# Kernel tuning notes

Measured on AMD Instinct MI355X. Metric: run time of the kernel, lower is better.

Reference implementation:

```python
import jax, jax.numpy as jnp
import numpy as np

N = 50000
E = 800000
C = 64
NEG_SLOPE = 0.2


def gat_conv(x, edge_index, W, att_src, att_dst, bias, heads, out_ch):
    """PyG GATConv forward (concat=True, add_self_loops=True).
    x: [N, in], edge_index: [2, E] (row0=src j, row1=dst i),
    W: [in, heads*out_ch], att_src/att_dst: [heads, out_ch], bias: [heads*out_ch].
    """
    n = x.shape[0]
    loop = jnp.arange(n, dtype=edge_index.dtype)
    src = jnp.concatenate([edge_index[0], loop])
    dst = jnp.concatenate([edge_index[1], loop])

    xl = (x @ W).reshape(n, heads, out_ch)            # [N, H, F]
    a_src = jnp.einsum('nhf,hf->nh', xl, att_src)      # [N, H]
    a_dst = jnp.einsum('nhf,hf->nh', xl, att_dst)      # [N, H]

    alpha = jax.nn.leaky_relu(a_src[src] + a_dst[dst], NEG_SLOPE)  # [E', H]
    # segment softmax over incoming edges of each destination node
    amax = jax.ops.segment_max(alpha, dst, num_segments=n)
    alpha = jnp.exp(alpha - amax[dst])
    denom = jax.ops.segment_sum(alpha, dst, num_segments=n)
    alpha = alpha / denom[dst]

    # gather source features, weight, scatter-add to destinations
    msg = xl[src] * alpha[:, :, None]                  # [E', H, F]
    out = jax.ops.segment_sum(msg, dst, num_segments=n)  # [N, H, F]
    return out.reshape(n, heads * out_ch) + bias


def setup_inputs() -> dict:
    key = jax.random.key(0)
    ks = jax.random.split(key, 12)
    x = jax.random.normal(ks[0], (N, C), dtype=jnp.float32)
    undirected = jax.random.randint(ks[1], (2, E), 0, N, dtype=jnp.int32)
    directed = jax.random.randint(ks[2], (2, E), 0, N, dtype=jnp.int32)

    s1 = 1.0 / np.sqrt(C)
    s2 = 1.0 / np.sqrt(2 * C)
    W1 = jax.random.normal(ks[3], (C, 2 * C), dtype=jnp.float32) * s1
    att_src1 = jax.random.normal(ks[4], (2, C), dtype=jnp.float32) * s1
    att_dst1 = jax.random.normal(ks[5], (2, C), dtype=jnp.float32) * s1
    b1 = jnp.zeros((2 * C,), dtype=jnp.float32)

    W2 = jax.random.normal(ks[6], (2 * C, 4 * C), dtype=jnp.float32) * s2
    att_src2 = jax.random.normal(ks[7], (2, 2 * C), dtype=jnp.float32) * s2
    att_dst2 = jax.random.normal(ks[8], (2, 2 * C), dtype=jnp.float32) * s2
    b2 = jnp.zeros((4 * C,), dtype=jnp.float32)

    return {
        'x': x,
        'undirected_edges_small': undirected,
        'directed_edges_small': directed,
        'W1': W1, 'att_src1': att_src1, 'att_dst1': att_dst1, 'b1': b1,
        'W2': W2, 'att_src2': att_src2, 'att_dst2': att_dst2, 'b2': b2,
    }


def reference(x, undirected_edges_small, directed_edges_small,
              W1, att_src1, att_dst1, b1,
              W2, att_src2, att_dst2, b2):
    h = gat_conv(x, undirected_edges_small, W1, att_src1, att_dst1, b1,
                 heads=2, out_ch=C)            # [N, 2C]
    out = gat_conv(h, directed_edges_small, W2, att_src2, att_dst2, b2,
                   heads=2, out_ch=2 * C)      # [N, 4C]
    return out
```

## Files before the change

### kernel.cpp

```cpp
#include <hip/hip_runtime.h>
#include <stdint.h>

#define N_NODES 50000
#define N_EDGES 800000
#define CAP 64
#define NBUCK 400
#define BSZ 125
#define BCAP 2816
#define LOG2E 1.4426950408889634f

typedef __attribute__((ext_vector_type(8))) short bf16x8;
typedef __attribute__((ext_vector_type(4))) float f32x4;

__device__ __forceinline__ float b2f_bits(unsigned int lo16) {
    union { unsigned int i; float f; } v; v.i = lo16 << 16; return v.f;
}
__device__ __forceinline__ unsigned short f2b(float f) {
    union { float f; unsigned int i; } v; v.f = f;
    unsigned int x = v.i;
    return (unsigned short)((x + 0x7fffu + ((x >> 16) & 1u)) >> 16);
}
__device__ __forceinline__ void split2(float v, unsigned short& h, unsigned short& l) {
    h = f2b(v);
    l = f2b(v - b2f_bits(h));
}
__device__ __forceinline__ void unpack8(const uint4 u, float* f) {
    f[0] = b2f_bits(u.x & 0xffffu); f[1] = b2f_bits(u.x >> 16);
    f[2] = b2f_bits(u.y & 0xffffu); f[3] = b2f_bits(u.y >> 16);
    f[4] = b2f_bits(u.z & 0xffffu); f[5] = b2f_bits(u.z >> 16);
    f[6] = b2f_bits(u.w & 0xffffu); f[7] = b2f_bits(u.w >> 16);
}
__device__ __forceinline__ void pack8hl(const float* v, uint4& H, uint4& L) {
    unsigned short h[8], l[8];
#pragma unroll
    for (int k = 0; k < 8; ++k) split2(v[k], h[k], l[k]);
    H.x = h[0] | ((unsigned)h[1] << 16); H.y = h[2] | ((unsigned)h[3] << 16);
    H.z = h[4] | ((unsigned)h[5] << 16); H.w = h[6] | ((unsigned)h[7] << 16);
    L.x = l[0] | ((unsigned)l[1] << 16); L.y = l[2] | ((unsigned)l[3] << 16);
    L.z = l[4] | ((unsigned)l[5] << 16); L.w = l[6] | ((unsigned)l[7] << 16);
}

__global__ __launch_bounds__(256) void proj_kernel(
    const float* __restrict__ W1, const float* __restrict__ as1, const float* __restrict__ ad1,
    const float* __restrict__ b1,
    const float* __restrict__ W2, const float* __restrict__ as2, const float* __restrict__ ad2,
    float* __restrict__ P1, float* __restrict__ q2, float* __restrict__ cs,
    int* __restrict__ gcur)
{
    for (int i = threadIdx.x; i < 2 * NBUCK + 2; i += 256) gcur[i] = 0;

    __shared__ float p2[4 * 128];
    for (int i = threadIdx.x; i < 4 * 128; i += 256) {
        const int t = i >> 7, c = i & 127;
        const int h = t & 1;
        const float* att = (t < 2) ? as2 : ad2;
        float s = 0.f;
        for (int cc = 0; cc < 128; ++cc)
            s += att[h * 128 + cc] * W2[(size_t)c * 256 + h * 128 + cc];
        p2[i] = s;
    }
    {
        const int t = threadIdx.x >> 6, k = threadIdx.x & 63;
        const int h = t & 1;
        const float* att = (t < 2) ? as1 : ad1;
        float s = 0.f;
        for (int c = 0; c < 64; ++c)
            s += att[h * 64 + c] * W1[(size_t)k * 128 + h * 64 + c];
        P1[t * 64 + k] = s * LOG2E;
    }
    __syncthreads();
    for (int i = threadIdx.x; i < 4 * 128; i += 256) {
        const int t = i >> 7, j = i & 127;
        const int hc = j >> 6, k = j & 63;
        float s = 0.f;
        for (int c = 0; c < 64; ++c)
            s += W1[(size_t)k * 128 + hc * 64 + c] * p2[t * 128 + hc * 64 + c];
        q2[i] = s * LOG2E;
    }
    if (threadIdx.x < 4) {
        const int t = threadIdx.x;
        float s = 0.f;
        for (int c = 0; c < 128; ++c) s += b1[c] * p2[t * 128 + c];
        cs[t] = s * LOG2E;
    }
}

__global__ __launch_bounds__(256) void prep1_kernel(
    const float* __restrict__ X, const float* __restrict__ P1,
    const float* __restrict__ W1, const float* __restrict__ W2,
    unsigned short* __restrict__ Xh,
    float* __restrict__ a_src, float* __restrict__ a_dst,
    unsigned short* __restrict__ w1h, unsigned short* __restrict__ w1l,
    unsigned short* __restrict__ w2h, unsigned short* __restrict__ w2l,
    float* __restrict__ att2buf, int n)
{
    const int bid = blockIdx.x;
    if (bid < 128) {
        const int i = bid * 256 + threadIdx.x;
        const int nn = i >> 7, k = i & 127;
        unsigned short h, l;
        split2(W2[(size_t)k * 256 + nn], h, l);
        w2h[i] = h; w2l[i] = l;
        return;
    }
    if (bid < 160) {
        const int i = (bid - 128) * 256 + threadIdx.x;
        const int nn = i >> 6, k = i & 63;
        unsigned short h, l;
        split2(W1[(size_t)k * 128 + nn], h, l);
        w1h[i] = h; w1l[i] = l;
        return;
    }
    const int gid = (bid - 160) * 256 + threadIdx.x;
    if (gid < n) ((float4*)att2buf)[gid] = make_float4(0.f, 0.f, 0.f, 0.f);
    const int node = gid >> 4;
    const int sl = threadIdx.x & 15;
    if (node >= n) return;
    const float4 v = *(const float4*)(X + (size_t)node * 64 + sl * 4);
    ushort4 hv;
    hv.x = f2b(v.x); hv.y = f2b(v.y); hv.z = f2b(v.z); hv.w = f2b(v.w);
    *(ushort4*)(Xh + (size_t)node * 64 + sl * 4) = hv;
    float d[4];
#pragma unroll
    for (int t = 0; t < 4; ++t) {
        const float* pp = P1 + t * 64 + sl * 4;
        d[t] = v.x * pp[0] + v.y * pp[1] + v.z * pp[2] + v.w * pp[3];
    }
#pragma unroll
    for (int o = 1; o < 16; o <<= 1)
#pragma unroll
        for (int t = 0; t < 4; ++t) d[t] += __shfl_xor(d[t], o);
    if (sl == 0) {
        *(float2*)(a_src + node * 2) = make_float2(d[0], d[1]);
        *(float2*)(a_dst + node * 2) = make_float2(d[2], d[3]);
    }
}

__global__ __launch_bounds__(256) void bucket_kernel(
    const int* __restrict__ e1, const int* __restrict__ e2, int ne,
    int* __restrict__ gcur, unsigned int* __restrict__ stage)
{
    const int layer = blockIdx.x & 1;
    const int bslot = blockIdx.x >> 1;
    const int nbl = gridDim.x >> 1;
    const int* __restrict__ eix = layer ? e2 : e1;
    int* cur = gcur + layer * NBUCK;
    unsigned int* __restrict__ stg = stage + (size_t)layer * NBUCK * BCAP;

    __shared__ int cnt_lds[NBUCK];
    __shared__ int base_lds[NBUCK];
    constexpr int EPT = 16;
    constexpr int CHUNK = 256 * EPT;

    for (int base = bslot * CHUNK; base < ne; base += nbl * CHUNK) {
        for (int i = threadIdx.x; i < NBUCK; i += 256) cnt_lds[i] = 0;
        __syncthreads();

        unsigned int rec[EPT];
        int bk[EPT];
#pragma unroll
        for (int i = 0; i < EPT; ++i) {
            const int e = base + i * 256 + threadIdx.x;
            bk[i] = -1;
            if (e < ne) {
                const int s = eix[e];
                const int d = eix[ne + e];
                if ((unsigned)d < (unsigned)N_NODES) {
                    const int b = d / BSZ;
                    bk[i] = b;
                    rec[i] = (unsigned)s | ((unsigned)(d - b * BSZ) << 16);
                    atomicAdd(&cnt_lds[b], 1);
                }
            }
        }
        __syncthreads();
        for (int i = threadIdx.x; i < NBUCK; i += 256) {
            const int c = cnt_lds[i];
            base_lds[i] = c ? atomicAdd(&cur[i], c) : 0;
            cnt_lds[i] = 0;
        }
        __syncthreads();
#pragma unroll
        for (int i = 0; i < EPT; ++i) {
            if (bk[i] >= 0) {
                const int idx = base_lds[bk[i]] + atomicAdd(&cnt_lds[bk[i]], 1);
                if (idx < BCAP) stg[(size_t)bk[i] * BCAP + idx] = rec[i];
            }
        }
        __syncthreads();
    }
}

__global__ __launch_bounds__(256) void place_kernel(
    const unsigned int* __restrict__ stage, const int* __restrict__ gcur,
    int* __restrict__ gtot,
    unsigned int* __restrict__ offs1, unsigned int* __restrict__ offs2,
    unsigned short* __restrict__ ss1, unsigned short* __restrict__ ss2)
{
    const int layer = blockIdx.x & 1;
    const int bucket = blockIdx.x >> 1;
    int m = gcur[layer * NBUCK + bucket];
    m = m < BCAP ? m : BCAP;
    const unsigned int* __restrict__ stg =
        stage + ((size_t)(layer * NBUCK + bucket)) * BCAP;
    unsigned int* __restrict__ offs = layer ? offs2 : offs1;
    unsigned short* __restrict__ ss = layer ? ss2 : ss1;
    const int d0 = bucket * BSZ;

    __shared__ int c_lds[BSZ];
    __shared__ int pref[BSZ + 1];
    __shared__ int baseSh;
    __shared__ unsigned short img[BCAP];

    for (int i = threadIdx.x; i < BSZ; i += 256) c_lds[i] = 0;
    __syncthreads();

    for (int i = threadIdx.x; i < m; i += 256)
        atomicAdd(&c_lds[stg[i] >> 16], 1);
    __syncthreads();

    if (threadIdx.x == 0) {
        int run = 0;
        for (int i = 0; i < BSZ; ++i) {
            int c = c_lds[i]; c = c < CAP ? c : CAP;
            pref[i] = run; run += c;
        }
        pref[BSZ] = run;
        baseSh = atomicAdd(&gtot[layer], run);
    }
    __syncthreads();
    const int base = baseSh;
    for (int i = threadIdx.x; i < BSZ; i += 256) {
        int c = c_lds[i]; c = c < CAP ? c : CAP;
        offs[d0 + i] = ((unsigned)(base + pref[i]) << 7) | (unsigned)c;
        c_lds[i] = 0;
    }
    __syncthreads();

    for (int i = threadIdx.x; i < m; i += 256) {
        const unsigned int v = stg[i];
        const int dr = (int)(v >> 16);
        const int slot = atomicAdd(&c_lds[dr], 1);
        if (slot < CAP) img[pref[dr] + slot] = (unsigned short)(v & 0xffffu);
    }
    __syncthreads();

    unsigned short* out = ss + base;
    const int tot = pref[BSZ];
    for (int i = threadIdx.x; i < tot; i += 256) out[i] = img[i];
}

__global__ __launch_bounds__(256) void agg1_kernel(
    const unsigned short* __restrict__ XH, const float* __restrict__ X,
    const float* __restrict__ a_src, const float* __restrict__ a_dst,
    const unsigned int* __restrict__ offs, const unsigned short* __restrict__ bins,
    unsigned short* __restrict__ AH, unsigned short* __restrict__ AL, int n)
{
    const int node = (blockIdx.x * 256 + threadIdx.x) >> 6;
    const int lane = threadIdx.x & 63;
    if (node >= n) return;
    const int hl = lane & 7;
    const int sub = lane >> 3;

    const unsigned o = offs[node];
    const int start = (int)(o >> 7);
    const int deg = (int)(o & 127);
    const int e = start + deg;
    const float2 ad = *(const float2*)(a_dst + node * 2);

    float2 As; float4 sva, svb;
    if (sub == 0) {
        As = *(const float2*)(a_src + node * 2);
        sva = *(const float4*)(X + (size_t)node * 64 + hl * 8);
        svb = *(const float4*)(X + (size_t)node * 64 + hl * 8 + 4);
    }

    float acc0[8] = {0.f,0.f,0.f,0.f,0.f,0.f,0.f,0.f};
    float acc1[8] = {0.f,0.f,0.f,0.f,0.f,0.f,0.f,0.f};
    float den0 = 0.f, den1 = 0.f;

    int p = start;
    int jc = 0; float2 Ac = make_float2(0.f, 0.f); uint4 uc = make_uint4(0,0,0,0);
    if (p < e) {
        const int pos = p + sub;
        const int pc = pos < e ? pos : e - 1;
        jc = bins[pc];
        Ac = *(const float2*)(a_src + jc * 2);
        uc = *(const uint4*)(XH + (size_t)jc * 64 + hl * 8);
    }
    while (p < e) {
        const int pn = p + 8;
        int jn = 0; float2 An; uint4 un;
        const bool more = pn < e;
        if (more) {
            const int pos = pn + sub;
            const int pc = pos < e ? pos : e - 1;
            jn = bins[pc];
            An = *(const float2*)(a_src + jn * 2);
            un = *(const uint4*)(XH + (size_t)jn * 64 + hl * 8);
        }
        float l0 = Ac.x + ad.x; l0 = fmaxf(l0, 0.2f * l0);
        float l1 = Ac.y + ad.y; l1 = fmaxf(l1, 0.2f * l1);
        float w0 = __builtin_amdgcn_exp2f(l0);
        float w1 = __builtin_amdgcn_exp2f(l1);
        if (p + sub >= e) { w0 = 0.f; w1 = 0.f; }
        den0 += w0; den1 += w1;
        float f[8]; unpack8(uc, f);
#pragma unroll
        for (int k = 0; k < 8; ++k) { acc0[k] += w0 * f[k]; acc1[k] += w1 * f[k]; }
        if (!more) break;
        jc = jn; Ac = An; uc = un; p = pn;
    }
    if (sub == 0) {
        float l0 = As.x + ad.x; l0 = fmaxf(l0, 0.2f * l0);
        float l1 = As.y + ad.y; l1 = fmaxf(l1, 0.2f * l1);
        const float w0 = __builtin_amdgcn_exp2f(l0);
        const float w1 = __builtin_amdgcn_exp2f(l1);
        den0 += w0; den1 += w1;
        float f[8] = {sva.x, sva.y, sva.z, sva.w, svb.x, svb.y, svb.z, svb.w};
#pragma unroll
        for (int k = 0; k < 8; ++k) { acc0[k] += w0 * f[k]; acc1[k] += w1 * f[k]; }
    }
#pragma unroll
    for (int o2 = 8; o2 < 64; o2 <<= 1) {
        den0 += __shfl_xor(den0, o2); den1 += __shfl_xor(den1, o2);
#pragma unroll
        for (int k = 0; k < 8; ++k) {
            acc0[k] += __shfl_xor(acc0[k], o2);
            acc1[k] += __shfl_xor(acc1[k], o2);
        }
    }
    if (sub < 2) {
        const int head = sub;
        const float inv = 1.f / (head ? den1 : den0);
        float vv[8];
#pragma unroll
        for (int k = 0; k < 8; ++k) vv[k] = (head ? acc1[k] : acc0[k]) * inv;
        uint4 H, L;
        pack8hl(vv, H, L);
        const size_t off = (size_t)head * N_NODES * 64 + (size_t)node * 64 + hl * 8;
        *(uint4*)(AH + off) = H;
        *(uint4*)(AL + off) = L;
    }
}

__global__ __launch_bounds__(256) void agg2_kernel(
    const unsigned short* __restrict__ HH, const unsigned short* __restrict__ HL,
    const float* __restrict__ a_src, const float* __restrict__ a_dst,
    const float* __restrict__ cs,
    const unsigned int* __restrict__ offs, const unsigned short* __restrict__ bins,
    unsigned short* __restrict__ AH, unsigned short* __restrict__ AL, int n)
{
    const int node = (blockIdx.x * 256 + threadIdx.x) >> 6;
    const int lane = threadIdx.x & 63;
    if (node >= n) return;
    const int hl = lane & 15;
    const int sub = lane >> 4;

    const float4 csv = *(const float4*)cs;
    const float C0 = csv.x + csv.z, C1 = csv.y + csv.w;

    const unsigned o = offs[node];
    const int start = (int)(o >> 7);
    const int deg = (int)(o & 127);
    const int e = start + deg;
    const float2 ad = *(const float2*)(a_dst + node * 2);
    const float ad0 = ad.x + C0, ad1 = ad.y + C1;

    float2 As; uint4 suh, sul;
    if (sub == 0) {
        As = *(const float2*)(a_src + node * 2);
        suh = *(const uint4*)(HH + (size_t)node * 128 + hl * 8);
        sul = *(const uint4*)(HL + (size_t)node * 128 + hl * 8);
    }

    float acc0[8] = {0.f,0.f,0.f,0.f,0.f,0.f,0.f,0.f};
    float acc1[8] = {0.f,0.f,0.f,0.f,0.f,0.f,0.f,0.f};
    float den0 = 0.f, den1 = 0.f;

    int p = start;
    int jc = 0; float2 Ac = make_float2(0.f, 0.f); uint4 uc = make_uint4(0,0,0,0);
    if (p < e) {
        const int pos = p + sub;
        const int pc = pos < e ? pos : e - 1;
        jc = bins[pc];
        Ac = *(const float2*)(a_src + jc * 2);
        uc = *(const uint4*)(HH + (size_t)jc * 128 + hl * 8);
    }
    while (p < e) {
        const int pn = p + 4;
        int jn = 0; float2 An; uint4 un;
        const bool more = pn < e;
        if (more) {
            const int pos = pn + sub;
            const int pc = pos < e ? pos : e - 1;
            jn = bins[pc];
            An = *(const float2*)(a_src + jn * 2);
            un = *(const uint4*)(HH + (size_t)jn * 128 + hl * 8);
        }
        float l0 = Ac.x + ad0; l0 = fmaxf(l0, 0.2f * l0);
        float l1 = Ac.y + ad1; l1 = fmaxf(l1, 0.2f * l1);
        float w0 = __builtin_amdgcn_exp2f(l0);
        float w1 = __builtin_amdgcn_exp2f(l1);
        if (p + sub >= e) { w0 = 0.f; w1 = 0.f; }
        den0 += w0; den1 += w1;
        float f[8]; unpack8(uc, f);
#pragma unroll
        for (int k = 0; k < 8; ++k) { acc0[k] += w0 * f[k]; acc1[k] += w1 * f[k]; }
        if (!more) break;
        jc = jn; Ac = An; uc = un; p = pn;
    }
    if (sub == 0) {
        float l0 = As.x + ad0; l0 = fmaxf(l0, 0.2f * l0);
        float l1 = As.y + ad1; l1 = fmaxf(l1, 0.2f * l1);
        const float w0 = __builtin_amdgcn_exp2f(l0);
        const float w1 = __builtin_amdgcn_exp2f(l1);
        den0 += w0; den1 += w1;
        float fh[8], fl[8];
        unpack8(suh, fh); unpack8(sul, fl);
#pragma unroll
        for (int k = 0; k < 8; ++k) {
            const float f = fh[k] + fl[k];
            acc0[k] += w0 * f; acc1[k] += w1 * f;
        }
    }
#pragma unroll
    for (int o2 = 16; o2 < 64; o2 <<= 1) {
        den0 += __shfl_xor(den0, o2); den1 += __shfl_xor(den1, o2);
#pragma unroll
        for (int k = 0; k < 8; ++k) {
            acc0[k] += __shfl_xor(acc0[k], o2);
            acc1[k] += __shfl_xor(acc1[k], o2);
        }
    }
    if (sub < 2) {
        const int head = sub;
        const float inv = 1.f / (head ? den1 : den0);
        float vv[8];
#pragma unroll
        for (int k = 0; k < 8; ++k) vv[k] = (head ? acc1[k] : acc0[k]) * inv;
        uint4 H, L;
        pack8hl(vv, H, L);
        const size_t off = (size_t)head * N_NODES * 128 + (size_t)node * 128 + hl * 8;
        *(uint4*)(AH + off) = H;
        *(uint4*)(AL + off) = L;
    }
}

__global__ __launch_bounds__(512) void gemm_h_kernel(
    const unsigned short* __restrict__ AH, const unsigned short* __restrict__ AL,
    const unsigned short* __restrict__ WTh, const unsigned short* __restrict__ WTl,
    const float* __restrict__ b1, const float* __restrict__ q2,
    unsigned short* __restrict__ HH, unsigned short* __restrict__ HL,
    float* __restrict__ a_src2, float* __restrict__ a_dst2, int M)
{
    constexpr int K = 64, KC = 2;
    const int wave = threadIdx.x >> 6;
    const int lane = threadIdx.x & 63;
    const int head = wave >> 2;
    const int c0 = (wave & 3) * 16;
    const int lr = lane & 15;
    const int lk = (lane >> 4) * 8;
    const int colg = head * 64 + c0 + ((lane >> 4) << 2);
    const bool doAtt = (wave & 3) == 0;

    bf16x8 awh[KC], awl[KC];
    {
        const unsigned short* wr  = WTh + (size_t)(head * 64 + c0 + lr) * K + lk;
        const unsigned short* wr2 = WTl + (size_t)(head * 64 + c0 + lr) * K + lk;
#pragma unroll
        for (int c = 0; c < KC; ++c) {
            awh[c] = *(const bf16x8*)(wr + c * 32);
            awl[c] = *(const bf16x8*)(wr2 + c * 32);
        }
    }
    const float4 bias = *(const float4*)(b1 + colg);
    const unsigned short* XhB = AH + (size_t)head * M * 64;
    const unsigned short* XlB = AL + (size_t)head * M * 64;

    auto loadB = [&](bf16x8 (&bh)[KC], bf16x8 (&bl)[KC], int sidx) {
        const unsigned short* xr  = XhB + (size_t)(sidx * 16 + lr) * 64 + lk;
        const unsigned short* xr2 = XlB + (size_t)(sidx * 16 + lr) * 64 + lk;
#pragma unroll
        for (int c = 0; c < KC; ++c) {
            bh[c] = *(const bf16x8*)(xr + c * 32);
            bl[c] = *(const bf16x8*)(xr2 + c * 32);
        }
    };
    auto compute = [&](bf16x8 (&bh)[KC], bf16x8 (&bl)[KC], int sidx) {
        f32x4 acc = {0.f, 0.f, 0.f, 0.f};
#pragma unroll
        for (int c = 0; c < KC; ++c)
            acc = __builtin_amdgcn_mfma_f32_16x16x32_bf16(awh[c], bh[c], acc, 0, 0, 0);
#pragma unroll
        for (int c = 0; c < KC; ++c)
            acc = __builtin_amdgcn_mfma_f32_16x16x32_bf16(awh[c], bl[c], acc, 0, 0, 0);
#pragma unroll
        for (int c = 0; c < KC; ++c)
            acc = __builtin_amdgcn_mfma_f32_16x16x32_bf16(awl[c], bh[c], acc, 0, 0, 0);
        ushort4 hv, lv;
        split2(acc[0] + bias.x, hv.x, lv.x); split2(acc[1] + bias.y, hv.y, lv.y);
        split2(acc[2] + bias.z, hv.z, lv.z); split2(acc[3] + bias.w, hv.w, lv.w);
        const size_t o = (size_t)(sidx * 16 + lr) * 128 + colg;
        *(ushort4*)(HH + o) = hv;
        *(ushort4*)(HL + o) = lv;
        if (doAtt) {
            float P[4] = {0.f, 0.f, 0.f, 0.f};
#pragma unroll
            for (int c = 0; c < KC; ++c)
#pragma unroll
                for (int i = 0; i < 8; ++i) {
                    const float v = b2f_bits((unsigned short)bh[c][i])
                                  + b2f_bits((unsigned short)bl[c][i]);
                    const int kk = head * 64 + lk + c * 32 + i;
#pragma unroll
                    for (int t = 0; t < 4; ++t) P[t] += v * q2[t * 128 + kk];
                }
#pragma unroll
            for (int o2 = 16; o2 < 64; o2 <<= 1)
#pragma unroll
                for (int t = 0; t < 4; ++t) P[t] += __shfl_xor(P[t], o2);
            if (lane < 16) {
                const int m = sidx * 16 + lane;
                atomicAdd(&a_src2[m * 2 + 0], P[0]);
                atomicAdd(&a_src2[m * 2 + 1], P[1]);
                atomicAdd(&a_dst2[m * 2 + 0], P[2]);
                atomicAdd(&a_dst2[m * 2 + 1], P[3]);
            }
        }
    };

    const int NSTRIP = M / 16;
    const int nb = gridDim.x;
    int s = blockIdx.x;
    bf16x8 b0h[KC], b0l[KC], b1h_[KC], b1l_[KC];
    if (s < NSTRIP) loadB(b0h, b0l, s);
    while (s < NSTRIP) {
        const int sn = s + nb;
        if (sn < NSTRIP) loadB(b1h_, b1l_, sn);
        compute(b0h, b0l, s);
        if (sn >= NSTRIP) break;
        const int sn2 = sn + nb;
        if (sn2 < NSTRIP) loadB(b0h, b0l, sn2);
        compute(b1h_, b1l_, sn);
        s = sn2;
    }
}

__global__ __launch_bounds__(512) void gemm_out_kernel(
    const unsigned short* __restrict__ AH, const unsigned short* __restrict__ AL,
    const unsigned short* __restrict__ WTh, const unsigned short* __restrict__ WTl,
    const float* __restrict__ b2,
    float* __restrict__ OUT, int M)
{
    constexpr int K = 128, KC = 4, CT = 2;
    const int wave = threadIdx.x >> 6;
    const int lane = threadIdx.x & 63;
    const int head = wave >> 2;
    const int c0 = (wave & 3) * 32;
    const int lr = lane & 15;
    const int lk = (lane >> 4) * 8;

    bf16x8 awh[CT][KC], awl[CT][KC];
    float4 bias[CT];
    int colg[CT];
#pragma unroll
    for (int t = 0; t < CT; ++t) {
        const unsigned short* wr  = WTh + (size_t)(head * 128 + c0 + t * 16 + lr) * K + lk;
        const unsigned short* wr2 = WTl + (size_t)(head * 128 + c0 + t * 16 + lr) * K + lk;
#pragma unroll
        for (int c = 0; c < KC; ++c) {
            awh[t][c] = *(const bf16x8*)(wr + c * 32);
            awl[t][c] = *(const bf16x8*)(wr2 + c * 32);
        }
        colg[t] = head * 128 + c0 + t * 16 + ((lane >> 4) << 2);
        bias[t] = *(const float4*)(b2 + colg[t]);
    }
    const unsigned short* XhB = AH + (size_t)head * M * 128;
    const unsigned short* XlB = AL + (size_t)head * M * 128;

    auto loadB = [&](bf16x8 (&bh)[KC], bf16x8 (&bl)[KC], int sidx) {
        const unsigned short* xr  = XhB + (size_t)(sidx * 16 + lr) * 128 + lk;
        const unsigned short* xr2 = XlB + (size_t)(sidx * 16 + lr) * 128 + lk;
#pragma unroll
        for (int c = 0; c < KC; ++c) {
            bh[c] = *(const bf16x8*)(xr + c * 32);
            bl[c] = *(const bf16x8*)(xr2 + c * 32);
        }
    };
    auto compute = [&](bf16x8 (&bh)[KC], bf16x8 (&bl)[KC], int sidx) {
#pragma unroll
        for (int t = 0; t < CT; ++t) {
            f32x4 acc = {0.f, 0.f, 0.f, 0.f};
#pragma unroll
            for (int c = 0; c < KC; ++c)
                acc = __builtin_amdgcn_mfma_f32_16x16x32_bf16(awh[t][c], bh[c], acc, 0, 0, 0);
#pragma unroll
            for (int c = 0; c < KC; ++c)
                acc = __builtin_amdgcn_mfma_f32_16x16x32_bf16(awh[t][c], bl[c], acc, 0, 0, 0);
#pragma unroll
            for (int c = 0; c < KC; ++c)
                acc = __builtin_amdgcn_mfma_f32_16x16x32_bf16(awl[t][c], bh[c], acc, 0, 0, 0);
            float4 o;
            o.x = acc[0] + bias[t].x; o.y = acc[1] + bias[t].y;
            o.z = acc[2] + bias[t].z; o.w = acc[3] + bias[t].w;
            *(float4*)(OUT + (size_t)(sidx * 16 + lr) * 256 + colg[t]) = o;
        }
    };

    const int NSTRIP = M / 16;
    const int nb = gridDim.x;
    int s = blockIdx.x;
    bf16x8 b0h[KC], b0l[KC], b1h_[KC], b1l_[KC];
    if (s < NSTRIP) loadB(b0h, b0l, s);
    while (s < NSTRIP) {
        const int sn = s + nb;
        if (sn < NSTRIP) loadB(b1h_, b1l_, sn);
        compute(b0h, b0l, s);
        if (sn >= NSTRIP) break;
        const int sn2 = sn + nb;
        if (sn2 < NSTRIP) loadB(b0h, b0l, sn2);
        compute(b1h_, b1l_, sn);
        s = sn2;
    }
}

extern "C" void kernel_launch(void* const* d_in, const int* in_sizes, int n_in,
                              void* d_out, int out_size, void* d_ws, size_t ws_size,
                              hipStream_t stream)
{
    const int N = N_NODES, E = N_EDGES;

    const float* x   = (const float*)d_in[0];
    const int*   und = (const int*)d_in[1];
    const int*   dir = (const int*)d_in[2];
    const float* W1  = (const float*)d_in[3];
    const float* as1 = (const float*)d_in[4];
    const float* ad1 = (const float*)d_in[5];
    const float* b1  = (const float*)d_in[6];
    const float* W2  = (const float*)d_in[7];
    const float* as2 = (const float*)d_in[8];
    const float* ad2 = (const float*)d_in[9];
    const float* b2  = (const float*)d_in[10];

    char* p = (char*)d_ws;
    auto alloc = [&](size_t bytes) {
        char* r = p;
        p += (bytes + 255) & ~(size_t)255;
        return r;
    };
    unsigned short* agg2h = (unsigned short*)alloc((size_t)2 * N * 128 * 2);
    unsigned short* agg2l = (unsigned short*)alloc((size_t)2 * N * 128 * 2);
    unsigned short* hhbuf = (unsigned short*)alloc((size_t)N * 128 * 2);
    unsigned short* hlbuf = (unsigned short*)alloc((size_t)N * 128 * 2);
    unsigned short* ss1   = (unsigned short*)alloc((size_t)E * 2);
    unsigned short* ss2   = (unsigned short*)alloc((size_t)E * 2);
    unsigned int* offs1 = (unsigned int*)alloc((size_t)N * 4);
    unsigned int* offs2 = (unsigned int*)alloc((size_t)N * 4);
    float* a_src1 = (float*)alloc((size_t)N * 2 * 4);
    float* a_dst1 = (float*)alloc((size_t)N * 2 * 4);
    float* att2buf = (float*)alloc((size_t)N * 4 * 4);
    int*   gcur  = (int*)alloc(((size_t)2 * NBUCK + 2) * 4);
    unsigned short* w1th = (unsigned short*)alloc((size_t)128 * 64 * 2);
    unsigned short* w1tl = (unsigned short*)alloc((size_t)128 * 64 * 2);
    unsigned short* w2th = (unsigned short*)alloc((size_t)256 * 128 * 2);
    unsigned short* w2tl = (unsigned short*)alloc((size_t)256 * 128 * 2);
    float* P1d = (float*)alloc(4 * 64 * 4);
    float* q2d = (float*)alloc(4 * 128 * 4);
    float* csd = (float*)alloc(4 * 4);
    int* gtot = gcur + 2 * NBUCK;
    float* a_src2 = att2buf, * a_dst2 = att2buf + (size_t)N * 2;

    unsigned int* stage = (unsigned int*)agg2h;
    unsigned short* x1h   = (unsigned short*)d_out;
    unsigned short* agg1h = (unsigned short*)d_out + (size_t)N * 64;
    unsigned short* agg1l = (unsigned short*)d_out + (size_t)N * 64 + (size_t)N * 128;

    const int WB = (N * 64) / 256;

    proj_kernel<<<1, 256, 0, stream>>>(W1, as1, ad1, b1, W2, as2, ad2,
                                       P1d, q2d, csd, gcur);
    bucket_kernel<<<2 * 196, 256, 0, stream>>>(und, dir, E, gcur, stage);
    place_kernel<<<2 * NBUCK, 256, 0, stream>>>(stage, gcur, gtot,
                                                offs1, offs2, ss1, ss2);
    prep1_kernel<<<160 + (N * 16) / 256, 256, 0, stream>>>(
        x, P1d, W1, W2, x1h, a_src1, a_dst1,
        w1th, w1tl, w2th, w2tl, att2buf, N);

    agg1_kernel<<<WB, 256, 0, stream>>>(x1h, x, a_src1, a_dst1, offs1, ss1,
                                        agg1h, agg1l, N);
    gemm_h_kernel<<<768, 512, 0, stream>>>(agg1h, agg1l, w1th, w1tl, b1, q2d,
                                           hhbuf, hlbuf, a_src2, a_dst2, N);

    agg2_kernel<<<WB, 256, 0, stream>>>(hhbuf, hlbuf, a_src2, a_dst2, csd,
                                        offs2, ss2, agg2h, agg2l, N);
    gemm_out_kernel<<<512, 512, 0, stream>>>(agg2h, agg2l, w2th, w2tl, b2,
                                             (float*)d_out, N);
}
```

Baseline: 295.8 us.

## Fuse edge aggregation with following MFMA GEMM via LDS staging per strip

Replaces the separate aggregation and GEMM kernels for both GAT layers with fused kernels. Each 512-thread block handles 16-node strips: waves aggregate two nodes each, write the hi/lo bf16 split results into swizzled LDS, then apply the weight transform with MFMA and write outputs directly. This removes the global round trip of the aggregated intermediates and two launches. In exchange it drops the software prefetch in the gather loop, adds two block barriers per strip, and moves the staging buffer to its own workspace allocation.

```diff
diff --git a/kernel.cpp b/kernel.cpp
--- a/kernel.cpp
+++ b/kernel.cpp
@@ -250,378 +250,283 @@
     for (int i = threadIdx.x; i < tot; i += 256) out[i] = img[i];
 }
 
-__global__ __launch_bounds__(256) void agg1_kernel(
+__global__ __launch_bounds__(512, 4) void fused1_kernel(
     const unsigned short* __restrict__ XH, const float* __restrict__ X,
     const float* __restrict__ a_src, const float* __restrict__ a_dst,
     const unsigned int* __restrict__ offs, const unsigned short* __restrict__ bins,
-    unsigned short* __restrict__ AH, unsigned short* __restrict__ AL, int n)
-{
-    const int node = (blockIdx.x * 256 + threadIdx.x) >> 6;
+    const unsigned short* __restrict__ WTh, const unsigned short* __restrict__ WTl,
+    const float* __restrict__ b1, const float* __restrict__ q2,
+    unsigned short* __restrict__ HH, unsigned short* __restrict__ HL,
+    float* __restrict__ a_src2, float* __restrict__ a_dst2, int nstrips)
+{
+    __shared__ __align__(16) unsigned char lds[2 * 2 * 16 * 128];
+    const int wave = threadIdx.x >> 6;
     const int lane = threadIdx.x & 63;
-    if (node >= n) return;
     const int hl = lane & 7;
     const int sub = lane >> 3;
-
-    const unsigned o = offs[node];
-    const int start = (int)(o >> 7);
-    const int deg = (int)(o & 127);
-    const int e = start + deg;
-    const float2 ad = *(const float2*)(a_dst + node * 2);
-
-    float2 As; float4 sva, svb;
-    if (sub == 0) {
-        As = *(const float2*)(a_src + node * 2);
-        sva = *(const float4*)(X + (size_t)node * 64 + hl * 8);
-        svb = *(const float4*)(X + (size_t)node * 64 + hl * 8 + 4);
-    }
-
-    float acc0[8] = {0.f,0.f,0.f,0.f,0.f,0.f,0.f,0.f};
-    float acc1[8] = {0.f,0.f,0.f,0.f,0.f,0.f,0.f,0.f};
-    float den0 = 0.f, den1 = 0.f;
-
-    int p = start;
-    int jc = 0; float2 Ac = make_float2(0.f, 0.f); uint4 uc = make_uint4(0,0,0,0);
-    if (p < e) {
-        const int pos = p + sub;
-        const int pc = pos < e ? pos : e - 1;
-        jc = bins[pc];
-        Ac = *(const float2*)(a_src + jc * 2);
-        uc = *(const uint4*)(XH + (size_t)jc * 64 + hl * 8);
-    }
-    while (p < e) {
-        const int pn = p + 8;
-        int jn = 0; float2 An; uint4 un;
-        const bool more = pn < e;
-        if (more) {
-            const int pos = pn + sub;
-            const int pc = pos < e ? pos : e - 1;
-            jn = bins[pc];
-            An = *(const float2*)(a_src + jn * 2);
-            un = *(const uint4*)(XH + (size_t)jn * 64 + hl * 8);
-        }
-        float l0 = Ac.x + ad.x; l0 = fmaxf(l0, 0.2f * l0);
-        float l1 = Ac.y + ad.y; l1 = fmaxf(l1, 0.2f * l1);
-        float w0 = __builtin_amdgcn_exp2f(l0);
-        float w1 = __builtin_amdgcn_exp2f(l1);
-        if (p + sub >= e) { w0 = 0.f; w1 = 0.f; }
-        den0 += w0; den1 += w1;
-        float f[8]; unpack8(uc, f);
-#pragma unroll
-        for (int k = 0; k < 8; ++k) { acc0[k] += w0 * f[k]; acc1[k] += w1 * f[k]; }
-        if (!more) break;
-        jc = jn; Ac = An; uc = un; p = pn;
-    }
-    if (sub == 0) {
-        float l0 = As.x + ad.x; l0 = fmaxf(l0, 0.2f * l0);
-        float l1 = As.y + ad.y; l1 = fmaxf(l1, 0.2f * l1);
-        const float w0 = __builtin_amdgcn_exp2f(l0);
-        const float w1 = __builtin_amdgcn_exp2f(l1);
-        den0 += w0; den1 += w1;
-        float f[8] = {sva.x, sva.y, sva.z, sva.w, svb.x, svb.y, svb.z, svb.w};
-#pragma unroll
-        for (int k = 0; k < 8; ++k) { acc0[k] += w0 * f[k]; acc1[k] += w1 * f[k]; }
-    }
-#pragma unroll
-    for (int o2 = 8; o2 < 64; o2 <<= 1) {
-        den0 += __shfl_xor(den0, o2); den1 += __shfl_xor(den1, o2);
-#pragma unroll
-        for (int k = 0; k < 8; ++k) {
-            acc0[k] += __shfl_xor(acc0[k], o2);
-            acc1[k] += __shfl_xor(acc1[k], o2);
-        }
-    }
-    if (sub < 2) {
-        const int head = sub;
-        const float inv = 1.f / (head ? den1 : den0);
-        float vv[8];
-#pragma unroll
-        for (int k = 0; k < 8; ++k) vv[k] = (head ? acc1[k] : acc0[k]) * inv;
-        uint4 H, L;
-        pack8hl(vv, H, L);
-        const size_t off = (size_t)head * N_NODES * 64 + (size_t)node * 64 + hl * 8;
-        *(uint4*)(AH + off) = H;
-        *(uint4*)(AL + off) = L;
-    }
-}
-
-__global__ __launch_bounds__(256) void agg2_kernel(
+    const int headC = wave >> 2;
+    const int c0 = (wave & 3) * 16;
+    const int lr = lane & 15;
+    const int lk = (lane >> 4) * 8;
+    const int colg = headC * 64 + c0 + ((lane >> 4) << 2);
+    const bool doAtt = (wave & 3) == 0;
+
+    bf16x8 awh[2], awl[2];
+    {
+        const unsigned short* wr  = WTh + (size_t)(headC * 64 + c0 + lr) * 64 + lk;
+        const unsigned short* wr2 = WTl + (size_t)(headC * 64 + c0 + lr) * 64 + lk;
+        awh[0] = *(const bf16x8*)(wr);  awh[1] = *(const bf16x8*)(wr + 32);
+        awl[0] = *(const bf16x8*)(wr2); awl[1] = *(const bf16x8*)(wr2 + 32);
+    }
+    const float4 bias = *(const float4*)(b1 + colg);
+
+    for (int strip = blockIdx.x; strip < nstrips; strip += gridDim.x) {
+#pragma unroll
+        for (int nn = 0; nn < 2; ++nn) {
+            const int node = strip * 16 + wave * 2 + nn;
+            const int ln = wave * 2 + nn;
+            const unsigned o = offs[node];
+            const int start = (int)(o >> 7);
+            const int e = start + (int)(o & 127);
+            const float2 ad = *(const float2*)(a_dst + node * 2);
+            float acc0[8] = {0,0,0,0,0,0,0,0}, acc1[8] = {0,0,0,0,0,0,0,0};
+            float den0 = 0.f, den1 = 0.f;
+            for (int p = start; p < e; p += 8) {
+                const int pos = p + sub;
+                const int pc = pos < e ? pos : e - 1;
+                const int j = bins[pc];
+                const float2 A = *(const float2*)(a_src + j * 2);
+                const uint4 u = *(const uint4*)(XH + (size_t)j * 64 + hl * 8);
+                float l0 = A.x + ad.x; l0 = fmaxf(l0, 0.2f * l0);
+                float l1 = A.y + ad.y; l1 = fmaxf(l1, 0.2f * l1);
+                float w0 = __builtin_amdgcn_exp2f(l0);
+                float w1 = __builtin_amdgcn_exp2f(l1);
+                if (pos >= e) { w0 = 0.f; w1 = 0.f; }
+                den0 += w0; den1 += w1;
+                float f[8]; unpack8(u, f);
+#pragma unroll
+                for (int k = 0; k < 8; ++k) { acc0[k] += w0 * f[k]; acc1[k] += w1 * f[k]; }
+            }
+            if (sub == 0) {
+                const float2 A = *(const float2*)(a_src + node * 2);
+                const float4 va = *(const float4*)(X + (size_t)node * 64 + hl * 8);
+                const float4 vb = *(const float4*)(X + (size_t)node * 64 + hl * 8 + 4);
+                float l0 = A.x + ad.x; l0 = fmaxf(l0, 0.2f * l0);
+                float l1 = A.y + ad.y; l1 = fmaxf(l1, 0.2f * l1);
+                const float w0 = __builtin_amdgcn_exp2f(l0);
+                const float w1 = __builtin_amdgcn_exp2f(l1);
+                den0 += w0; den1 += w1;
+                float f[8] = {va.x, va.y, va.z, va.w, vb.x, vb.y, vb.z, vb.w};
+#pragma unroll
+                for (int k = 0; k < 8; ++k) { acc0[k] += w0 * f[k]; acc1[k] += w1 * f[k]; }
+            }
+#pragma unroll
+            for (int o2 = 8; o2 < 64; o2 <<= 1) {
+                den0 += __shfl_xor(den0, o2); den1 += __shfl_xor(den1, o2);
+#pragma unroll
+                for (int k = 0; k < 8; ++k) {
+                    acc0[k] += __shfl_xor(acc0[k], o2);
+                    acc1[k] += __shfl_xor(acc1[k], o2);
+                }
+            }
+            if (sub < 2) {
+                const float inv = 1.f / (sub ? den1 : den0);
+                float vv[8];
+#pragma unroll
+                for (int k = 0; k < 8; ++k) vv[k] = (sub ? acc1[k] : acc0[k]) * inv;
+                uint4 H, L;
+                pack8hl(vv, H, L);
+                const int b = (hl * 16) ^ ((ln & 7) << 4);
+                *(uint4*)(lds + ((0 * 2 + sub) * 16 + ln) * 128 + b) = H;
+                *(uint4*)(lds + ((1 * 2 + sub) * 16 + ln) * 128 + b) = L;
+            }
+        }
+        __syncthreads();
+        {
+            bf16x8 bh[2], bl[2];
+#pragma unroll
+            for (int c = 0; c < 2; ++c) {
+                const int b = ((lk + c * 32) * 2) ^ ((lr & 7) << 4);
+                bh[c] = *(const bf16x8*)(lds + ((0 * 2 + headC) * 16 + lr) * 128 + b);
+                bl[c] = *(const bf16x8*)(lds + ((1 * 2 + headC) * 16 + lr) * 128 + b);
+            }
+            f32x4 acc = {0.f, 0.f, 0.f, 0.f};
+#pragma unroll
+            for (int c = 0; c < 2; ++c)
+                acc = __builtin_amdgcn_mfma_f32_16x16x32_bf16(awh[c], bh[c], acc, 0, 0, 0);
+#pragma unroll
+            for (int c = 0; c < 2; ++c)
+                acc = __builtin_amdgcn_mfma_f32_16x16x32_bf16(awh[c], bl[c], acc, 0, 0, 0);
+#pragma unroll
+            for (int c = 0; c < 2; ++c)
+                acc = __builtin_amdgcn_mfma_f32_16x16x32_bf16(awl[c], bh[c], acc, 0, 0, 0);
+            ushort4 hv, lv;
+            split2(acc[0] + bias.x, hv.x, lv.x); split2(acc[1] + bias.y, hv.y, lv.y);
+            split2(acc[2] + bias.z, hv.z, lv.z); split2(acc[3] + bias.w, hv.w, lv.w);
+            const size_t og = (size_t)(strip * 16 + lr) * 128 + colg;
+            *(ushort4*)(HH + og) = hv;
+            *(ushort4*)(HL + og) = lv;
+            if (doAtt) {
+                float P[4] = {0.f, 0.f, 0.f, 0.f};
+#pragma unroll
+                for (int c = 0; c < 2; ++c)
+#pragma unroll
+                    for (int i = 0; i < 8; ++i) {
+                        const float v = b2f_bits((unsigned short)bh[c][i])
+                                      + b2f_bits((unsigned short)bl[c][i]);
+                        const int kk = headC * 64 + lk + c * 32 + i;
+#pragma unroll
+                        for (int t = 0; t < 4; ++t) P[t] += v * q2[t * 128 + kk];
+                    }
+#pragma unroll
+                for (int o2 = 16; o2 < 64; o2 <<= 1)
+#pragma unroll
+                    for (int t = 0; t < 4; ++t) P[t] += __shfl_xor(P[t], o2);
+                if (lane < 16) {
+                    const int m = strip * 16 + lane;
+                    atomicAdd(&a_src2[m * 2 + 0], P[0]);
+                    atomicAdd(&a_src2[m * 2 + 1], P[1]);
+                    atomicAdd(&a_dst2[m * 2 + 0], P[2]);
+                    atomicAdd(&a_dst2[m * 2 + 1], P[3]);
+                }
+            }
+        }
+        __syncthreads();
+    }
+}
+
+__global__ __launch_bounds__(512, 4) void fused2_kernel(
     const unsigned short* __restrict__ HH, const unsigned short* __restrict__ HL,
     const float* __restrict__ a_src, const float* __restrict__ a_dst,
     const float* __restrict__ cs,
     const unsigned int* __restrict__ offs, const unsigned short* __restrict__ bins,
-    unsigned short* __restrict__ AH, unsigned short* __restrict__ AL, int n)
-{
-    const int node = (blockIdx.x * 256 + threadIdx.x) >> 6;
+    const unsigned short* __restrict__ WTh, const unsigned short* __restrict__ WTl,
+    const float* __restrict__ b2,
+    float* __restrict__ OUT, int nstrips)
+{
+    __shared__ __align__(16) unsigned char lds[2 * 2 * 16 * 256];
+    const int wave = threadIdx.x >> 6;
     const int lane = threadIdx.x & 63;
-    if (node >= n) return;
     const int hl = lane & 15;
     const int sub = lane >> 4;
-
-    const float4 csv = *(const float4*)cs;
-    const float C0 = csv.x + csv.z, C1 = csv.y + csv.w;
-
-    const unsigned o = offs[node];
-    const int start = (int)(o >> 7);
-    const int deg = (int)(o & 127);
-    const int e = start + deg;
-    const float2 ad = *(const float2*)(a_dst + node * 2);
-    const float ad0 = ad.x + C0, ad1 = ad.y + C1;
-
-    float2 As; uint4 suh, sul;
-    if (sub == 0) {
-        As = *(const float2*)(a_src + node * 2);
-        suh = *(const uint4*)(HH + (size_t)node * 128 + hl * 8);
-        sul = *(const uint4*)(HL + (size_t)node * 128 + hl * 8);
-    }
-
-    float acc0[8] = {0.f,0.f,0.f,0.f,0.f,0.f,0.f,0.f};
-    float acc1[8] = {0.f,0.f,0.f,0.f,0.f,0.f,0.f,0.f};
-    float den0 = 0.f, den1 = 0.f;
-
-    int p = start;
-    int jc = 0; float2 Ac = make_float2(0.f, 0.f); uint4 uc = make_uint4(0,0,0,0);
-    if (p < e) {
-        const int pos = p + sub;
-        const int pc = pos < e ? pos : e - 1;
-        jc = bins[pc];
-        Ac = *(const float2*)(a_src + jc * 2);
-        uc = *(const uint4*)(HH + (size_t)jc * 128 + hl * 8);
-    }
-    while (p < e) {
-        const int pn = p + 4;
-        int jn = 0; float2 An; uint4 un;
-        const bool more = pn < e;
-        if (more) {
-            const int pos = pn + sub;
-            const int pc = pos < e ? pos : e - 1;
-            jn = bins[pc];
-            An = *(const float2*)(a_src + jn * 2);
-            un = *(const uint4*)(HH + (size_t)jn * 128 + hl * 8);
-        }
-        float l0 = Ac.x + ad0; l0 = fmaxf(l0, 0.2f * l0);
-        float l1 = Ac.y + ad1; l1 = fmaxf(l1, 0.2f * l1);
-        float w0 = __builtin_amdgcn_exp2f(l0);
-        float w1 = __builtin_amdgcn_exp2f(l1);
-        if (p + sub >= e) { w0 = 0.f; w1 = 0.f; }
-        den0 += w0; den1 += w1;
-        float f[8]; unpack8(uc, f);
-#pragma unroll
-        for (int k = 0; k < 8; ++k) { acc0[k] += w0 * f[k]; acc1[k] += w1 * f[k]; }
-        if (!more) break;
-        jc = jn; Ac = An; uc = un; p = pn;
-    }
-    if (sub == 0) {
-        float l0 = As.x + ad0; l0 = fmaxf(l0, 0.2f * l0);
-        float l1 = As.y + ad1; l1 = fmaxf(l1, 0.2f * l1);
-        const float w0 = __builtin_amdgcn_exp2f(l0);
-        const float w1 = __builtin_amdgcn_exp2f(l1);
-        den0 += w0; den1 += w1;
-        float fh[8], fl[8];
-        unpack8(suh, fh); unpack8(sul, fl);
-#pragma unroll
-        for (int k = 0; k < 8; ++k) {
-            const float f = fh[k] + fl[k];
-            acc0[k] += w0 * f; acc1[k] += w1 * f;
-        }
-    }
-#pragma unroll
-    for (int o2 = 16; o2 < 64; o2 <<= 1) {
-        den0 += __shfl_xor(den0, o2); den1 += __shfl_xor(den1, o2);
-#pragma unroll
-        for (int k = 0; k < 8; ++k) {
-            acc0[k] += __shfl_xor(acc0[k], o2);
-            acc1[k] += __shfl_xor(acc1[k], o2);
-        }
-    }
-    if (sub < 2) {
-        const int head = sub;
-        const float inv = 1.f / (head ? den1 : den0);
-        float vv[8];
-#pragma unroll
-        for (int k = 0; k < 8; ++k) vv[k] = (head ? acc1[k] : acc0[k]) * inv;
-        uint4 H, L;
-        pack8hl(vv, H, L);
-        const size_t off = (size_t)head * N_NODES * 128 + (size_t)node * 128 + hl * 8;
-        *(uint4*)(AH + off) = H;
-        *(uint4*)(AL + off) = L;
-    }
-}
-
-__global__ __launch_bounds__(512) void gemm_h_kernel(
-    const unsigned short* __restrict__ AH, const unsigned short* __restrict__ AL,
-    const unsigned short* __restrict__ WTh, const unsigned short* __restrict__ WTl,
-    const float* __restrict__ b1, const float* __restrict__ q2,
-    unsigned short* __restrict__ HH, unsigned short* __restrict__ HL,
-    float* __restrict__ a_src2, float* __restrict__ a_dst2, int M)
-{
-    constexpr int K = 64, KC = 2;
-    const int wave = threadIdx.x >> 6;
-    const int lane = threadIdx.x & 63;
-    const int head = wave >> 2;
-    const int c0 = (wave & 3) * 16;
-    const int lr = lane & 15;
-    const int lk = (lane >> 4) * 8;
-    const int colg = head * 64 + c0 + ((lane >> 4) << 2);
-    const bool doAtt = (wave & 3) == 0;
-
-    bf16x8 awh[KC], awl[KC];
-    {
-        const unsigned short* wr  = WTh + (size_t)(head * 64 + c0 + lr) * K + lk;
-        const unsigned short* wr2 = WTl + (size_t)(head * 64 + c0 + lr) * K + lk;
-#pragma unroll
-        for (int c = 0; c < KC; ++c) {
-            awh[c] = *(const bf16x8*)(wr + c * 32);
-            awl[c] = *(const bf16x8*)(wr2 + c * 32);
-        }
-    }
-    const float4 bias = *(const float4*)(b1 + colg);
-    const unsigned short* XhB = AH + (size_t)head * M * 64;
-    const unsigned short* XlB = AL + (size_t)head * M * 64;
-
-    auto loadB = [&](bf16x8 (&bh)[KC], bf16x8 (&bl)[KC], int sidx) {
-        const unsigned short* xr  = XhB + (size_t)(sidx * 16 + lr) * 64 + lk;
-        const unsigned short* xr2 = XlB + (size_t)(sidx * 16 + lr) * 64 + lk;
-#pragma unroll
-        for (int c = 0; c < KC; ++c) {
-            bh[c] = *(const bf16x8*)(xr + c * 32);
-            bl[c] = *(const bf16x8*)(xr2 + c * 32);
-        }
-    };
-    auto compute = [&](bf16x8 (&bh)[KC], bf16x8 (&bl)[KC], int sidx) {
-        f32x4 acc = {0.f, 0.f, 0.f, 0.f};
-#pragma unroll
-        for (int c = 0; c < KC; ++c)
-            acc = __builtin_amdgcn_mfma_f32_16x16x32_bf16(awh[c], bh[c], acc, 0, 0, 0);
-#pragma unroll
-        for (int c = 0; c < KC; ++c)
-            acc = __builtin_amdgcn_mfma_f32_16x16x32_bf16(awh[c], bl[c], acc, 0, 0, 0);
-#pragma unroll
-        for (int c = 0; c < KC; ++c)
-            acc = __builtin_amdgcn_mfma_f32_16x16x32_bf16(awl[c], bh[c], acc, 0, 0, 0);
-        ushort4 hv, lv;
-        split2(acc[0] + bias.x, hv.x, lv.x); split2(acc[1] + bias.y, hv.y, lv.y);
-        split2(acc[2] + bias.z, hv.z, lv.z); split2(acc[3] + bias.w, hv.w, lv.w);
-        const size_t o = (size_t)(sidx * 16 + lr) * 128 + colg;
-        *(ushort4*)(HH + o) = hv;
-        *(ushort4*)(HL + o) = lv;
-        if (doAtt) {
-            float P[4] = {0.f, 0.f, 0.f, 0.f};
-#pragma unroll
-            for (int c = 0; c < KC; ++c)
-#pragma unroll
-                for (int i = 0; i < 8; ++i) {
-                    const float v = b2f_bits((unsigned short)bh[c][i])
-                                  + b2f_bits((unsigned short)bl[c][i]);
-                    const int kk = head * 64 + lk + c * 32 + i;
-#pragma unroll
-                    for (int t = 0; t < 4; ++t) P[t] += v * q2[t * 128 + kk];
-                }
-#pragma unroll
-            for (int o2 = 16; o2 < 64; o2 <<= 1)
-#pragma unroll
-                for (int t = 0; t < 4; ++t) P[t] += __shfl_xor(P[t], o2);
-            if (lane < 16) {
-                const int m = sidx * 16 + lane;
-                atomicAdd(&a_src2[m * 2 + 0], P[0]);
-                atomicAdd(&a_src2[m * 2 + 1], P[1]);
-                atomicAdd(&a_dst2[m * 2 + 0], P[2]);
-                atomicAdd(&a_dst2[m * 2 + 1], P[3]);
-            }
-        }
-    };
-
-    const int NSTRIP = M / 16;
-    const int nb = gridDim.x;
-    int s = blockIdx.x;
-    bf16x8 b0h[KC], b0l[KC], b1h_[KC], b1l_[KC];
-    if (s < NSTRIP) loadB(b0h, b0l, s);
-    while (s < NSTRIP) {
-        const int sn = s + nb;
-        if (sn < NSTRIP) loadB(b1h_, b1l_, sn);
-        compute(b0h, b0l, s);
-        if (sn >= NSTRIP) break;
-        const int sn2 = sn + nb;
-        if (sn2 < NSTRIP) loadB(b0h, b0l, sn2);
-        compute(b1h_, b1l_, sn);
-        s = sn2;
-    }
-}
-
-__global__ __launch_bounds__(512) void gemm_out_kernel(
-    const unsigned short* __restrict__ AH, const unsigned short* __restrict__ AL,
-    const unsigned short* __restrict__ WTh, const unsigned short* __restrict__ WTl,
-    const float* __restrict__ b2,
-    float* __restrict__ OUT, int M)
-{
-    constexpr int K = 128, KC = 4, CT = 2;
-    const int wave = threadIdx.x >> 6;
-    const int lane = threadIdx.x & 63;
-    const int head = wave >> 2;
+    const int headC = wave >> 2;
     const int c0 = (wave & 3) * 32;
     const int lr = lane & 15;
     const int lk = (lane >> 4) * 8;
 
-    bf16x8 awh[CT][KC], awl[CT][KC];
-    float4 bias[CT];
-    int colg[CT];
-#pragma unroll
-    for (int t = 0; t < CT; ++t) {
-        const unsigned short* wr  = WTh + (size_t)(head * 128 + c0 + t * 16 + lr) * K + lk;
-        const unsigned short* wr2 = WTl + (size_t)(head * 128 + c0 + t * 16 + lr) * K + lk;
-#pragma unroll
-        for (int c = 0; c < KC; ++c) {
+    const float4 csv = *(const float4*)cs;
+    const float C0 = csv.x + csv.z, C1 = csv.y + csv.w;
+
+    bf16x8 awh[2][4], awl[2][4];
+    float4 bias[2];
+    int colg[2];
+#pragma unroll
+    for (int t = 0; t < 2; ++t) {
+        const unsigned short* wr  = WTh + (size_t)(headC * 128 + c0 + t * 16 + lr) * 128 + lk;
+        const unsigned short* wr2 = WTl + (size_t)(headC * 128 + c0 + t * 16 + lr) * 128 + lk;
+#pragma unroll
+        for (int c = 0; c < 4; ++c) {
             awh[t][c] = *(const bf16x8*)(wr + c * 32);
             awl[t][c] = *(const bf16x8*)(wr2 + c * 32);
         }
-        colg[t] = head * 128 + c0 + t * 16 + ((lane >> 4) << 2);
+        colg[t] = headC * 128 + c0 + t * 16 + ((lane >> 4) << 2);
         bias[t] = *(const float4*)(b2 + colg[t]);
     }
-    const unsigned short* XhB = AH + (size_t)head * M * 128;
-    const unsigned short* XlB = AL + (size_t)head * M * 128;
-
-    auto loadB = [&](bf16x8 (&bh)[KC], bf16x8 (&bl)[KC], int sidx) {
-        const unsigned short* xr  = XhB + (size_t)(sidx * 16 + lr) * 128 + lk;
-        const unsigned short* xr2 = XlB + (size_t)(sidx * 16 + lr) * 128 + lk;
-#pragma unroll
-        for (int c = 0; c < KC; ++c) {
-            bh[c] = *(const bf16x8*)(xr + c * 32);
-            bl[c] = *(const bf16x8*)(xr2 + c * 32);
-        }
-    };
-    auto compute = [&](bf16x8 (&bh)[KC], bf16x8 (&bl)[KC], int sidx) {
-#pragma unroll
-        for (int t = 0; t < CT; ++t) {
-            f32x4 acc = {0.f, 0.f, 0.f, 0.f};
-#pragma unroll
-            for (int c = 0; c < KC; ++c)
-                acc = __builtin_amdgcn_mfma_f32_16x16x32_bf16(awh[t][c], bh[c], acc, 0, 0, 0);
-#pragma unroll
-            for (int c = 0; c < KC; ++c)
-                acc = __builtin_amdgcn_mfma_f32_16x16x32_bf16(awh[t][c], bl[c], acc, 0, 0, 0);
-#pragma unroll
-            for (int c = 0; c < KC; ++c)
-                acc = __builtin_amdgcn_mfma_f32_16x16x32_bf16(awl[t][c], bh[c], acc, 0, 0, 0);
-            float4 o;
-            o.x = acc[0] + bias[t].x; o.y = acc[1] + bias[t].y;
-            o.z = acc[2] + bias[t].z; o.w = acc[3] + bias[t].w;
-            *(float4*)(OUT + (size_t)(sidx * 16 + lr) * 256 + colg[t]) = o;
-        }
-    };
-
-    const int NSTRIP = M / 16;
-    const int nb = gridDim.x;
-    int s = blockIdx.x;
-    bf16x8 b0h[KC], b0l[KC], b1h_[KC], b1l_[KC];
-    if (s < NSTRIP) loadB(b0h, b0l, s);
-    while (s < NSTRIP) {
-        const int sn = s + nb;
-        if (sn < NSTRIP) loadB(b1h_, b1l_, sn);
-        compute(b0h, b0l, s);
-        if (sn >= NSTRIP) break;
-        const int sn2 = sn + nb;
-        if (sn2 < NSTRIP) loadB(b0h, b0l, sn2);
-        compute(b1h_, b1l_, sn);
-        s = sn2;
+
+    for (int strip = blockIdx.x; strip < nstrips; strip += gridDim.x) {
+#pragma unroll
+        for (int nn = 0; nn < 2; ++nn) {
+            const int node = strip * 16 + wave * 2 + nn;
+            const int ln = wave * 2 + nn;
+            const unsigned o = offs[node];
+            const int start = (int)(o >> 7);
+            const int e = start + (int)(o & 127);
+            const float2 ad = *(const float2*)(a_dst + node * 2);
+            const float ad0 = ad.x + C0, ad1 = ad.y + C1;
+            float acc0[8] = {0,0,0,0,0,0,0,0}, acc1[8] = {0,0,0,0,0,0,0,0};
+            float den0 = 0.f, den1 = 0.f;
+            for (int p = start; p < e; p += 4) {
+                const int pos = p + sub;
+                const int pc = pos < e ? pos : e - 1;
+                const int j = bins[pc];
+                const float2 A = *(const float2*)(a_src + j * 2);
+                const uint4 u = *(const uint4*)(HH + (size_t)j * 128 + hl * 8);
+                float l0 = A.x + ad0; l0 = fmaxf(l0, 0.2f * l0);
+                float l1 = A.y + ad1; l1 = fmaxf(l1, 0.2f * l1);
+                float w0 = __builtin_amdgcn_exp2f(l0);
+                float w1 = __builtin_amdgcn_exp2f(l1);
+                if (pos >= e) { w0 = 0.f; w1 = 0.f; }
+                den0 += w0; den1 += w1;
+                float f[8]; unpack8(u, f);
+#pragma unroll
+                for (int k = 0; k < 8; ++k) { acc0[k] += w0 * f[k]; acc1[k] += w1 * f[k]; }
+            }
+            if (sub == 0) {
+                const float2 A = *(const float2*)(a_src + node * 2);
+                const uint4 uh = *(const uint4*)(HH + (size_t)node * 128 + hl * 8);
+                const uint4 ul = *(const uint4*)(HL + (size_t)node * 128 + hl * 8);
+                float l0 = A.x + ad0; l0 = fmaxf(l0, 0.2f * l0);
+                float l1 = A.y + ad1; l1 = fmaxf(l1, 0.2f * l1);
+                const float w0 = __builtin_amdgcn_exp2f(l0);
+                const float w1 = __builtin_amdgcn_exp2f(l1);
+                den0 += w0; den1 += w1;
+                float fh[8], fl[8];
+                unpack8(uh, fh); unpack8(ul, fl);
+#pragma unroll
+                for (int k = 0; k < 8; ++k) {
+                    const float f = fh[k] + fl[k];
+                    acc0[k] += w0 * f; acc1[k] += w1 * f;
+                }
+            }
+#pragma unroll
+            for (int o2 = 16; o2 < 64; o2 <<= 1) {
+                den0 += __shfl_xor(den0, o2); den1 += __shfl_xor(den1, o2);
+#pragma unroll
+                for (int k = 0; k < 8; ++k) {
+                    acc0[k] += __shfl_xor(acc0[k], o2);
+                    acc1[k] += __shfl_xor(acc1[k], o2);
+                }
+            }
+            if (sub < 2) {
+                const float inv = 1.f / (sub ? den1 : den0);
+                float vv[8];
+#pragma unroll
+                for (int k = 0; k < 8; ++k) vv[k] = (sub ? acc1[k] : acc0[k]) * inv;
+                uint4 H, L;
+                pack8hl(vv, H, L);
+                const int b = (hl * 16) ^ ((ln & 7) << 4);
+                *(uint4*)(lds + ((0 * 2 + sub) * 16 + ln) * 256 + b) = H;
+                *(uint4*)(lds + ((1 * 2 + sub) * 16 + ln) * 256 + b) = L;
+            }
+        }
+        __syncthreads();
+        {
+            bf16x8 bh[4], bl[4];
+#pragma unroll
+            for (int c = 0; c < 4; ++c) {
+                const int b = ((lk + c * 32) * 2) ^ ((lr & 7) << 4);
+                bh[c] = *(const bf16x8*)(lds + ((0 * 2 + headC) * 16 + lr) * 256 + b);
+                bl[c] = *(const bf16x8*)(lds + ((1 * 2 + headC) * 16 + lr) * 256 + b);
+            }
+#pragma unroll
+            for (int t = 0; t < 2; ++t) {
+                f32x4 acc = {0.f, 0.f, 0.f, 0.f};
+#pragma unroll
+                for (int c = 0; c < 4; ++c)
+                    acc = __builtin_amdgcn_mfma_f32_16x16x32_bf16(awh[t][c], bh[c], acc, 0, 0, 0);
+#pragma unroll
+                for (int c = 0; c < 4; ++c)
+                    acc = __builtin_amdgcn_mfma_f32_16x16x32_bf16(awh[t][c], bl[c], acc, 0, 0, 0);
+#pragma unroll
+                for (int c = 0; c < 4; ++c)
+                    acc = __builtin_amdgcn_mfma_f32_16x16x32_bf16(awl[t][c], bh[c], acc, 0, 0, 0);
+                float4 o;
+                o.x = acc[0] + bias[t].x; o.y = acc[1] + bias[t].y;
+                o.z = acc[2] + bias[t].z; o.w = acc[3] + bias[t].w;
+                *(float4*)(OUT + (size_t)(strip * 16 + lr) * 256 + colg[t]) = o;
+            }
+        }
+        __syncthreads();
     }
 }
 
@@ -649,10 +554,9 @@
         p += (bytes + 255) & ~(size_t)255;
         return r;
     };
-    unsigned short* agg2h = (unsigned short*)alloc((size_t)2 * N * 128 * 2);
-    unsigned short* agg2l = (unsigned short*)alloc((size_t)2 * N * 128 * 2);
     unsigned short* hhbuf = (unsigned short*)alloc((size_t)N * 128 * 2);
     unsigned short* hlbuf = (unsigned short*)alloc((size_t)N * 128 * 2);
+    unsigned int*   stage = (unsigned int*)alloc((size_t)2 * NBUCK * BCAP * 4);
     unsigned short* ss1   = (unsigned short*)alloc((size_t)E * 2);
     unsigned short* ss2   = (unsigned short*)alloc((size_t)E * 2);
     unsigned int* offs1 = (unsigned int*)alloc((size_t)N * 4);
@@ -671,12 +575,9 @@
     int* gtot = gcur + 2 * NBUCK;
     float* a_src2 = att2buf, * a_dst2 = att2buf + (size_t)N * 2;
 
-    unsigned int* stage = (unsigned int*)agg2h;
-    unsigned short* x1h   = (unsigned short*)d_out;
-    unsigned short* agg1h = (unsigned short*)d_out + (size_t)N * 64;
-    unsigned short* agg1l = (unsigned short*)d_out + (size_t)N * 64 + (size_t)N * 128;
-
-    const int WB = (N * 64) / 256;
+    unsigned short* x1h = (unsigned short*)d_out;
+
+    const int NSTRIPS = N / 16;
 
     proj_kernel<<<1, 256, 0, stream>>>(W1, as1, ad1, b1, W2, as2, ad2,
                                        P1d, q2d, csd, gcur);
@@ -687,13 +588,11 @@
         x, P1d, W1, W2, x1h, a_src1, a_dst1,
         w1th, w1tl, w2th, w2tl, att2buf, N);
 
-    agg1_kernel<<<WB, 256, 0, stream>>>(x1h, x, a_src1, a_dst1, offs1, ss1,
-                                        agg1h, agg1l, N);
-    gemm_h_kernel<<<768, 512, 0, stream>>>(agg1h, agg1l, w1th, w1tl, b1, q2d,
-                                           hhbuf, hlbuf, a_src2, a_dst2, N);
-
-    agg2_kernel<<<WB, 256, 0, stream>>>(hhbuf, hlbuf, a_src2, a_dst2, csd,
-                                        offs2, ss2, agg2h, agg2l, N);
-    gemm_out_kernel<<<512, 512, 0, stream>>>(agg2h, agg2l, w2th, w2tl, b2,
-                                             (float*)d_out, N);
-}
+    fused1_kernel<<<1024, 512, 0, stream>>>(
+        x1h, x, a_src1, a_dst1, offs1, ss1, w1th, w1tl, b1, q2d,
+        hhbuf, hlbuf, a_src2, a_dst2, NSTRIPS);
+
+    fused2_kernel<<<1024, 512, 0, stream>>>(
+        hhbuf, hlbuf, a_src2, a_dst2, csd, offs2, ss2, w2th, w2tl, b2,
+        (float*)d_out, NSTRIPS);
+}
```

Result: slower. 342.5 us (+15.8%).
